# Kernel optimization log

Hardware: AMD Instinct MI355X
Metric: run time of the kernel (lower is better)

## Reference

```python
import jax, jax.numpy as jnp
import numpy as np

RRELU_SLOPE = (1.0 / 8.0 + 1.0 / 3.0) / 2.0  # F.rrelu eval-mode slope
DILATIONS = (1, 2, 4, 8)
HIDDEN_TEMP = 1.0
GUMBEL_TEMP = 0.1


def rrelu(x):
    return jnp.where(x >= 0, x, RRELU_SLOPE * x)


def conv1d(x, w, b, dilation):
    # x: [B, Cin, T], w: [Cout, Cin, K] -> [B, Cout, T'] (VALID, dilated)
    y = jax.lax.conv_general_dilated(
        x, w, window_strides=(1,), padding='VALID', rhs_dilation=(dilation,),
        dimension_numbers=('NCH', 'OIH', 'NCH'))
    return y + b[None, :, None]


def setup_inputs() -> dict:
    key = jax.random.key(0)
    ks = jax.random.split(key, 16)
    B, D, T, R = 8, 32, 4096, 8
    s = 0.05  # param scale for numerical stability
    inp = {
        'x': jax.random.normal(ks[0], (B, D, T), jnp.float32),
        'u': jax.random.uniform(ks[1], (B, T, R), jnp.float32, 1e-6, 1.0 - 1e-6),
        'conv_w0': jax.random.normal(ks[2], (128, D, 2), jnp.float32) * s,
        'conv_b0': jax.random.normal(ks[3], (128,), jnp.float32) * s,
        'conv_w1': jax.random.normal(ks[4], (128, 128, 2), jnp.float32) * s,
        'conv_b1': jax.random.normal(ks[5], (128,), jnp.float32) * s,
        'conv_w2': jax.random.normal(ks[6], (128, 128, 2), jnp.float32) * s,
        'conv_b2': jax.random.normal(ks[7], (128,), jnp.float32) * s,
        'conv_w3': jax.random.normal(ks[8], (R, 128, 2), jnp.float32) * s,
        'conv_b3': jax.random.normal(ks[9], (R,), jnp.float32) * s,
        'pw0': jax.random.normal(ks[10], (R, 256, 128), jnp.float32) * s,
        'pb0': jax.random.normal(ks[11], (R, 256), jnp.float32) * s,
        'pw1': jax.random.normal(ks[12], (R, 2 * D, 256), jnp.float32) * s,
        'pb1': jax.random.normal(ks[13], (R, 2 * D), jnp.float32) * s,
    }
    return inp


def reference(x, u, conv_w0, conv_b0, conv_w1, conv_b1, conv_w2, conv_b2,
              conv_w3, conv_b3, pw0, pb0, pw1, pb1):
    pad = sum(DILATIONS)  # causal left pad
    h = jnp.pad(x, ((0, 0), (0, 0), (pad, 0)))
    for w, b, d in ((conv_w0, conv_b0, DILATIONS[0]),
                    (conv_w1, conv_b1, DILATIONS[1]),
                    (conv_w2, conv_b2, DILATIONS[2])):
        h = rrelu(conv1d(h, w, b, d))
    pre = h  # [B, 128, T + dilations[-1]]
    h_vecs = rrelu(conv1d(pre, conv_w3, conv_b3, DILATIONS[3]))  # [B, R, T]
    pre = pre[:, :, DILATIONS[3]:]  # [B, 128, T]

    p = jax.nn.softmax(h_vecs / HIDDEN_TEMP, axis=1)  # [B, R, T]
    logits = jnp.log(p).transpose(0, 2, 1)  # [B, T, R]
    g = -jnp.log(-jnp.log(u))  # gumbel noise from uniform input
    gen_z = jax.nn.softmax((logits + g) / GUMBEL_TEMP, axis=-1).transpose(0, 2, 1)  # [B, R, T]

    # Fused mixture-of-experts dynamic linear: equal to materializing
    # einsum('brt,roi->boit') then contracting with pre, but avoids the huge tensor.
    params = (jnp.einsum('brt,roi,bit->bot', gen_z, pw0, pre)
              + jnp.einsum('brt,ro->bot', gen_z, pb0))
    # NOTE: original calls F.rrelu(params) without assignment -> no-op (kept faithful)
    params = (jnp.einsum('brt,roi,bit->bot', gen_z, pw1, params)
              + jnp.einsum('brt,ro->bot', gen_z, pb1))

    mus, sig = jnp.split(params, 2, axis=1)  # each [B, n_dims, T]
    sigmas = 0.5 + 0.5 * jnp.tanh(sig) + 0.001
    return mus, sigmas, gen_z
```

## Files before the change

kernel.cpp:

```cpp
#include <hip/hip_runtime.h>
#include <math.h>

typedef __attribute__((ext_vector_type(8))) short bf16x8;
typedef __attribute__((ext_vector_type(4))) float f32x4;
struct __align__(8)  us4 { unsigned short x,y,z,w; };
struct __align__(16) ui4 { unsigned x,y,z,w; };

#define SLOPE 0.2291666666666667f
constexpr int N0=4110, N1=4108, N2=4104, NX=4111;

__device__ __forceinline__ unsigned short f2bf(float f){
  unsigned u = __float_as_uint(f);
  u = (u + 0x7FFF + ((u>>16)&1)) >> 16;
  return (unsigned short)u;
}
__device__ __forceinline__ float bf2f(unsigned short h){
  return __uint_as_float(((unsigned)h)<<16);
}
__device__ __forceinline__ float rrelu(float v){ return v>=0.f ? v : v*SLOPE; }

__global__ __launch_bounds__(256) void prep_w(
  const float* __restrict__ w0, const float* __restrict__ w1, const float* __restrict__ w2,
  const float* __restrict__ pw0, const float* __restrict__ pw1,
  const float* __restrict__ pb0, const float* __restrict__ pb1,
  unsigned short* __restrict__ w0e, unsigned short* __restrict__ w1e, unsigned short* __restrict__ w2e,
  unsigned short* __restrict__ pw0b, unsigned short* __restrict__ pw1b,
  unsigned short* __restrict__ pb0e, unsigned short* __restrict__ pb1e)
{
  int idx = blockIdx.x*256 + threadIdx.x;
  if (idx < 8192){ int oc=idx>>6, k=idx&63, tap=k>>5, i=k&31;
    w0e[idx] = f2bf(w0[(oc*32+i)*2+tap]); return; }
  idx -= 8192;
  if (idx < 32768){ int oc=idx>>8, k=idx&255, tap=k>>7, i=k&127;
    w1e[idx] = f2bf(w1[(oc*128+i)*2+tap]); return; }
  idx -= 32768;
  if (idx < 32768){ int oc=idx>>8, k=idx&255, tap=k>>7, i=k&127;
    w2e[idx] = f2bf(w2[(oc*128+i)*2+tap]); return; }
  idx -= 32768;
  if (idx < 262144){ pw0b[idx] = f2bf(pw0[idx]); return; }
  idx -= 262144;
  if (idx < 131072){ pw1b[idx] = f2bf(pw1[idx]); return; }
  idx -= 131072;
  if (idx < 8192){ int o=idx>>5, r=idx&31; pb0e[idx] = r<8 ? f2bf(pb0[r*256+o]) : (unsigned short)0; return; }
  idx -= 8192;
  if (idx < 2048){ int o=idx>>5, r=idx&31; pb1e[idx] = r<8 ? f2bf(pb1[r*64+o]) : (unsigned short)0; return; }
}

__global__ __launch_bounds__(64) void prep_xt(const float* __restrict__ x,
                                              unsigned short* __restrict__ xt)
{
  __shared__ float s[32][64];
  const int b = blockIdx.y, j0 = blockIdx.x*64, l = threadIdx.x;
  #pragma unroll 4
  for (int i=0;i<32;i++){
    int p = j0 + l - 15;
    s[i][l] = (p>=0 && p<4096) ? x[((size_t)b*32+i)*4096+p] : 0.f;
  }
  __syncthreads();
  const int j = j0 + l;
  if (j < NX){
    unsigned tmp[16];
    #pragma unroll
    for (int q=0;q<16;q++)
      tmp[q] = (unsigned)f2bf(s[2*q][l]) | ((unsigned)f2bf(s[2*q+1][l])<<16);
    ui4* dst = (ui4*)(xt + ((size_t)b*NX + j)*32);
    #pragma unroll
    for (int q=0;q<4;q++){ ui4 v={tmp[4*q],tmp[4*q+1],tmp[4*q+2],tmp[4*q+3]}; dst[q]=v; }
  }
}

template<int IC, int DIL, int NIN, int NOUT>
__global__ __launch_bounds__(256) void conv_g(
    const unsigned short* __restrict__ act,
    const unsigned short* __restrict__ wgt,
    const float* __restrict__ bias,
    unsigned short* __restrict__ outp)
{
  constexpr int KT   = 2*IC;
  constexpr int NK   = KT/32;
  constexpr int NH   = (KT > 128) ? 2 : 1;
  constexpr int KPH  = KT / NH;
  constexpr int NKH  = KPH/32;
  constexpr int HRB  = KPH*2;
  constexpr int HCPR = HRB/16;
  __shared__ __align__(16) char wsm[64*HRB];
  __shared__ __align__(16) char outs[64*128];

  const int tid = threadIdx.x;
  const int b = blockIdx.z, ob = blockIdx.y, tb = blockIdx.x*64;
  const int o0g = ob*64;
  const int wid = tid>>6, l = tid&63, lo = l&15, hi = l>>4;

  bf16x8 bfr[NK];
  {
    const int tg = tb + wid*16 + lo;
    const int te = tg < NOUT ? tg : NOUT-1;
    #pragma unroll
    for (int kk=0;kk<NK;kk++){
      int k = kk*32 + hi*8;
      int tap = (k >= IC) ? 1 : 0;
      int off = k - tap*IC;
      bfr[kk] = *(const bf16x8*)(act + ((size_t)b*NIN + te + tap*DIL)*IC + off);
    }
  }

  f32x4 acc[4];
  #pragma unroll
  for (int m=0;m<4;m++) acc[m] = (f32x4){0.f,0.f,0.f,0.f};

  #pragma unroll
  for (int h=0; h<NH; ++h){
    __syncthreads();
    for (int c = tid; c < 64*HCPR; c += 256){
      int row = c / HCPR, cc = c % HCPR;
      ui4 v = *(const ui4*)((const char*)wgt + (size_t)(o0g+row)*KT*2 + h*HRB + cc*16);
      *(ui4*)(wsm + row*HRB + ((cc*16) ^ ((row&7)<<4))) = v;
    }
    __syncthreads();
    #pragma unroll
    for (int kk=0;kk<NKH;kk++){
      #pragma unroll
      for (int m=0;m<4;m++){
        int row = m*16 + lo;
        bf16x8 af = *(const bf16x8*)(wsm + row*HRB + ((kk*64+hi*16) ^ ((row&7)<<4)));
        acc[m] = __builtin_amdgcn_mfma_f32_16x16x32_bf16(af, bfr[h*NKH+kk], acc[m], 0,0,0);
      }
    }
  }
  __syncthreads();
  #pragma unroll
  for (int m=0;m<4;m++){
    const int ol = m*16 + hi*4;
    float b0v = bias[o0g+ol+0], b1v = bias[o0g+ol+1], b2v = bias[o0g+ol+2], b3v = bias[o0g+ol+3];
    int tl = wid*16 + lo;
    us4 v;
    v.x = f2bf(rrelu(acc[m][0] + b0v));
    v.y = f2bf(rrelu(acc[m][1] + b1v));
    v.z = f2bf(rrelu(acc[m][2] + b2v));
    v.w = f2bf(rrelu(acc[m][3] + b3v));
    *(us4*)(outs + tl*128 + ((ol*2) ^ ((tl&7)<<4))) = v;
  }
  __syncthreads();
  #pragma unroll
  for (int i=0;i<2;i++){
    int c = tid + i*256;
    int row = c>>3, cc = c&7;
    if (tb + row < NOUT){
      ui4 v = *(const ui4*)(outs + row*128 + ((cc*16) ^ ((row&7)<<4)));
      *(ui4*)(outp + ((size_t)b*NOUT + tb + row)*128 + o0g + cc*8) = v;
    }
  }
}

__global__ __launch_bounds__(64) void gumbel_g(
  const unsigned short* __restrict__ h2t,
  const float* __restrict__ w3, const float* __restrict__ b3,
  const float* __restrict__ u,
  float* __restrict__ genz,
  unsigned short* __restrict__ zt)
{
  __shared__ unsigned hs[72][66];
  const int b = blockIdx.y, t0 = blockIdx.x*64, l = threadIdx.x;
  const unsigned* src = (const unsigned*)(h2t + ((size_t)b*N2 + t0)*128);
  for (int e=l; e<72*64; e+=64) hs[e>>6][e&63] = src[e];
  __syncthreads();

  float acc[8];
  #pragma unroll
  for (int r=0;r<8;r++) acc[r]=b3[r];
  for (int i2=0;i2<64;i2++){
    unsigned a0 = hs[l][i2], a1 = hs[l+8][i2];
    float v00 = bf2f(a0&0xffff), v01 = bf2f(a0>>16);
    float v10 = bf2f(a1&0xffff), v11 = bf2f(a1>>16);
    const int i = 2*i2;
    #pragma unroll
    for (int r=0;r<8;r++){
      acc[r] = fmaf(w3[(r*128+i)*2],     v00, acc[r]);
      acc[r] = fmaf(w3[(r*128+i)*2+1],   v10, acc[r]);
      acc[r] = fmaf(w3[(r*128+i+1)*2],   v01, acc[r]);
      acc[r] = fmaf(w3[(r*128+i+1)*2+1], v11, acc[r]);
    }
  }
  float m = -1e30f;
  #pragma unroll
  for (int r=0;r<8;r++){ acc[r] = rrelu(acc[r]); m = fmaxf(m, acc[r]); }
  float s = 0.f;
  #pragma unroll
  for (int r=0;r<8;r++) s += __expf(acc[r]-m);
  const float lse = m + __logf(s);
  const int t = t0 + l;
  const float* ub = u + ((size_t)b*4096 + t)*8;
  float y[8], m2 = -1e30f;
  #pragma unroll
  for (int r=0;r<8;r++){
    float g = -__logf(-__logf(ub[r]));
    y[r] = (acc[r] - lse + g)*10.f;
    m2 = fmaxf(m2, y[r]);
  }
  float s2 = 0.f;
  #pragma unroll
  for (int r=0;r<8;r++){ y[r] = __expf(y[r]-m2); s2 += y[r]; }
  const float inv = 1.f/s2;
  #pragma unroll
  for (int r=0;r<8;r++){
    y[r] *= inv;
    genz[((size_t)b*8+r)*4096 + t] = y[r];
  }
  ui4 zp = { (unsigned)f2bf(y[0]) | ((unsigned)f2bf(y[1])<<16),
             (unsigned)f2bf(y[2]) | ((unsigned)f2bf(y[3])<<16),
             (unsigned)f2bf(y[4]) | ((unsigned)f2bf(y[5])<<16),
             (unsigned)f2bf(y[6]) | ((unsigned)f2bf(y[7])<<16) };
  ui4 zz = {0,0,0,0};
  ui4* zd = (ui4*)(zt + ((size_t)b*4096 + t)*32);
  zd[0]=zp; zd[1]=zz; zd[2]=zz; zd[3]=zz;
}

__global__ __launch_bounds__(256) void moe1_m(
  const unsigned short* __restrict__ h2t,
  const float* __restrict__ genz,
  const unsigned short* __restrict__ zt,
  const unsigned short* __restrict__ pw0b,
  const unsigned short* __restrict__ pb0e,
  unsigned short* __restrict__ hidt)
{
  __shared__ __align__(16) char pres[16384];
  __shared__ __align__(16) char outb[8192];
  __shared__ float zl[512];

  const int ob = blockIdx.x, b = blockIdx.z, tb = blockIdx.y*64;
  const int o0g = ob*64;
  const int tid = threadIdx.x;
  #pragma unroll
  for (int i=0;i<2;i++){
    int e = tid + i*256;
    zl[e] = genz[((size_t)b*8 + (e>>6))*4096 + tb + (e&63)];
  }
  {
    const char* src = (const char*)(h2t + ((size_t)b*N2 + tb + 8)*128);
    #pragma unroll
    for (int i=0;i<4;i++){
      int c = tid + i*256, row = c>>4, cc = c&15;
      ui4 v = *(const ui4*)(src + row*256 + cc*16);
      *(ui4*)(pres + row*256 + ((cc*16) ^ ((row&7)<<4))) = v;
    }
  }
  __syncthreads();

  const int wid = tid>>6, l = tid&63, lo = l&15, hi = l>>4;
  const int ow = o0g + wid*16;

  bf16x8 bfr[4][4];
  #pragma unroll
  for (int n=0;n<4;n++){
    int tl = n*16 + lo;
    #pragma unroll
    for (int kk=0;kk<4;kk++)
      bfr[n][kk] = *(const bf16x8*)(pres + tl*256 + ((kk*64 + hi*16) ^ ((tl&7)<<4)));
  }
  f32x4 acc[4];
  {
    bf16x8 pf = *(const bf16x8*)(pb0e + (size_t)(ow + lo)*32 + hi*8);
    #pragma unroll
    for (int n=0;n<4;n++){
      bf16x8 zf = *(const bf16x8*)(zt + ((size_t)b*4096 + tb + n*16 + lo)*32 + hi*8);
      acc[n] = __builtin_amdgcn_mfma_f32_16x16x32_bf16(pf, zf, (f32x4){0.f,0.f,0.f,0.f}, 0,0,0);
    }
  }

  const unsigned short* abase = pw0b + (size_t)(ow + lo)*128 + hi*8;
  bf16x8 A[4], An[4];
  #pragma unroll
  for (int kk=0;kk<4;kk++) A[kk] = *(const bf16x8*)(abase + kk*32);

  #pragma unroll
  for (int r=0;r<8;r++){
    if (r < 7){
      #pragma unroll
      for (int kk=0;kk<4;kk++)
        An[kk] = *(const bf16x8*)(abase + (size_t)(r+1)*32768 + kk*32);
    }
    f32x4 ar[4];
    #pragma unroll
    for (int n=0;n<4;n++) ar[n] = (f32x4){0.f,0.f,0.f,0.f};
    #pragma unroll
    for (int kk=0;kk<4;kk++)
      #pragma unroll
      for (int n=0;n<4;n++)
        ar[n] = __builtin_amdgcn_mfma_f32_16x16x32_bf16(A[kk], bfr[n][kk], ar[n], 0,0,0);
    #pragma unroll
    for (int n=0;n<4;n++){
      float zv = zl[r*64 + n*16 + lo];
      #pragma unroll
      for (int c2=0;c2<4;c2++)
        acc[n][c2] = fmaf(zv, ar[n][c2], acc[n][c2]);
    }
    if (r < 7){
      #pragma unroll
      for (int kk=0;kk<4;kk++) A[kk] = An[kk];
    }
  }

  #pragma unroll
  for (int n=0;n<4;n++){
    int tl = n*16 + lo;
    int ol2 = (wid*16 + hi*4)*2;
    us4 v;
    v.x=f2bf(acc[n][0]); v.y=f2bf(acc[n][1]); v.z=f2bf(acc[n][2]); v.w=f2bf(acc[n][3]);
    *(us4*)(outb + tl*128 + (ol2 ^ ((tl&7)<<4))) = v;
  }
  __syncthreads();
  #pragma unroll
  for (int i=0;i<2;i++){
    int c = tid + i*256, row = c>>3, cc = c&7;
    ui4 v = *(const ui4*)(outb + row*128 + ((cc*16) ^ ((row&7)<<4)));
    *(ui4*)(hidt + (((size_t)b*4 + ob)*4096 + tb + row)*64 + cc*8) = v;
  }
}

__global__ __launch_bounds__(512) void moe2_m(
  const unsigned short* __restrict__ hidt,
  const float* __restrict__ genz,
  const unsigned short* __restrict__ zt,
  const unsigned short* __restrict__ pw1b,
  const unsigned short* __restrict__ pb1e,
  float* __restrict__ out)
{
  __shared__ __align__(16) char smem[32768*2 + 4096];
  char* abuf0 = smem;
  char* abuf1 = smem + 32768;
  float* zl  = (float*)(smem + 65536);

  const int wg = blockIdx.x;
  const int b = wg >> 5, tb = (wg & 31) * 128;

  const int tid = threadIdx.x;
  #pragma unroll
  for (int i=0;i<2;i++){
    int e = tid + i*512;
    zl[e] = genz[((size_t)b*8 + (e>>7))*4096 + tb + (e&127)];
  }

  const int wid = tid>>6, l = tid&63, lo = l&15, hi = l>>4;
  const int tg = tb + wid*16 + lo;

  bf16x8 bfr[8];
  #pragma unroll
  for (int kk=0;kk<8;kk++)
    bfr[kk] = *(const bf16x8*)(hidt + (((size_t)b*4 + (kk>>1))*4096 + tg)*64 + (kk&1)*32 + hi*8);
  f32x4 acc[4];
  {
    bf16x8 zf = *(const bf16x8*)(zt + ((size_t)b*4096 + tg)*32 + hi*8);
    #pragma unroll
    for (int m=0;m<4;m++){
      bf16x8 pf = *(const bf16x8*)(pb1e + (size_t)(m*16 + lo)*32 + hi*8);
      acc[m] = __builtin_amdgcn_mfma_f32_16x16x32_bf16(pf, zf, (f32x4){0.f,0.f,0.f,0.f}, 0,0,0);
    }
  }

  {
    const char* src = (const char*)pw1b;
    #pragma unroll
    for (int i=0;i<4;i++){
      int c = tid + i*512, row = c>>5, cc = c&31;
      ui4 v = *(const ui4*)(src + row*512 + cc*16);
      *(ui4*)(abuf0 + row*512 + ((cc*16) ^ ((row&7)<<4))) = v;
    }
  }
  __syncthreads();

  #pragma unroll
  for (int r=0;r<8;r++){
    char* cur = (r&1) ? abuf1 : abuf0;
    char* nxt = (r&1) ? abuf0 : abuf1;
    ui4 stg[4];
    if (r < 7){
      const char* src = (const char*)(pw1b + (size_t)(r+1)*16384);
      #pragma unroll
      for (int i=0;i<4;i++){
        int c = tid + i*512;
        stg[i] = *(const ui4*)(src + (c>>5)*512 + (c&31)*16);
      }
    }
    f32x4 ar[4];
    #pragma unroll
    for (int m=0;m<4;m++) ar[m] = (f32x4){0.f,0.f,0.f,0.f};
    #pragma unroll
    for (int kk=0;kk<8;kk++){
      #pragma unroll
      for (int m=0;m<4;m++){
        int row = m*16 + lo;
        int kb  = kk*64 + hi*16;
        bf16x8 af = *(const bf16x8*)(cur + row*512 + (kb ^ ((row&7)<<4)));
        ar[m] = __builtin_amdgcn_mfma_f32_16x16x32_bf16(af, bfr[kk], ar[m], 0,0,0);
      }
    }
    float zv = zl[r*128 + wid*16 + lo];
    #pragma unroll
    for (int m=0;m<4;m++)
      #pragma unroll
      for (int c2=0;c2<4;c2++)
        acc[m][c2] = fmaf(zv, ar[m][c2], acc[m][c2]);
    if (r < 7){
      #pragma unroll
      for (int i=0;i<4;i++){
        int c = tid + i*512;
        *(ui4*)(nxt + (c>>5)*512 + (((c&31)*16) ^ (((c>>5)&7)<<4))) = stg[i];
      }
    }
    __syncthreads();
  }

  #pragma unroll
  for (int m=0;m<4;m++){
    #pragma unroll
    for (int c2=0;c2<4;c2++){
      int o = m*16 + hi*4 + c2;
      float v = acc[m][c2];
      if (o < 32)
        out[((size_t)b*32 + o)*4096 + tg] = v;
      else {
        float e = __expf(2.f*v);
        float th = 1.f - 2.f/(e+1.f);
        out[(size_t)1048576 + ((size_t)b*32 + (o-32))*4096 + tg] = 0.5f + 0.5f*th + 0.001f;
      }
    }
  }
}

extern "C" void kernel_launch(void* const* d_in, const int* in_sizes, int n_in,
                              void* d_out, int out_size, void* d_ws, size_t ws_size,
                              hipStream_t stream) {
  const float* x   = (const float*)d_in[0];
  const float* u   = (const float*)d_in[1];
  const float* w0  = (const float*)d_in[2];
  const float* b0  = (const float*)d_in[3];
  const float* w1  = (const float*)d_in[4];
  const float* b1  = (const float*)d_in[5];
  const float* w2  = (const float*)d_in[6];
  const float* b2  = (const float*)d_in[7];
  const float* w3  = (const float*)d_in[8];
  const float* b3  = (const float*)d_in[9];
  const float* pw0 = (const float*)d_in[10];
  const float* pb0 = (const float*)d_in[11];
  const float* pw1 = (const float*)d_in[12];
  const float* pb1 = (const float*)d_in[13];

  float* out  = (float*)d_out;
  float* genz = out + (size_t)2*8*32*4096;

  char* p = (char*)d_ws;
  unsigned short* xt   = (unsigned short*)p; p += 2104832;
  unsigned short* h0t  = (unsigned short*)p; p += 8417280;
  unsigned short* h1t  = (unsigned short*)p; p += 8413184;
  unsigned short* h2t  = (unsigned short*)p; p += 8404992;
  unsigned short* ztb  = (unsigned short*)p; p += 2097152;
  unsigned short* hidt = (unsigned short*)p; p += 16777216;
  unsigned short* w0e  = (unsigned short*)p; p += 16384;
  unsigned short* w1e  = (unsigned short*)p; p += 65536;
  unsigned short* w2e  = (unsigned short*)p; p += 65536;
  unsigned short* pw0b = (unsigned short*)p; p += 524288;
  unsigned short* pw1b = (unsigned short*)p; p += 262144;
  unsigned short* pb0e = (unsigned short*)p; p += 16384;
  unsigned short* pb1e = (unsigned short*)p; p += 4096;

  prep_w<<<1864, 256, 0, stream>>>(w0,w1,w2,pw0,pw1,pb0,pb1,
                                   w0e,w1e,w2e,pw0b,pw1b,pb0e,pb1e);
  prep_xt<<<dim3(65,8), 64, 0, stream>>>(x, xt);
  conv_g<32,1,NX,N0><<<dim3(65,2,8), 256, 0, stream>>>(xt,  w0e, b0, h0t);
  conv_g<128,2,N0,N1><<<dim3(65,2,8), 256, 0, stream>>>(h0t, w1e, b1, h1t);
  conv_g<128,4,N1,N2><<<dim3(65,2,8), 256, 0, stream>>>(h1t, w2e, b2, h2t);
  gumbel_g<<<dim3(64,8), 64, 0, stream>>>(h2t, w3, b3, u, genz, ztb);
  moe1_m<<<dim3(4,64,8), 256, 0, stream>>>(h2t, genz, ztb, pw0b, pb0e, hidt);
  moe2_m<<<256, 512, 0, stream>>>(hidt, genz, ztb, pw1b, pb1e, out);
}
```

Measured before the change: 132.4 us.

## Restructure moe2 to register-resident expert weights and LDS-staged activations

In moe1, expert-weight fragments are now double-buffered in registers with a distance-two prefetch, alternating between A0 and A1 instead of copying An to A. moe2 is reorganised the same way as moe1. Each wave now holds a 16-row slice of the pw1 expert weights in registers, with two-deep prefetch across experts, and the 64-timestep activation tile is staged once into swizzled LDS. This replaces the old scheme that streamed the full per-expert weight matrix through double-buffered LDS with a barrier every expert. The grid becomes 512 blocks of 256 threads rather than 256 of 512, and the per-expert syncthreads go away. The cost is higher register pressure (16 bf16x8 weight fragments per thread) and repeated LDS reads of activations for every expert.

```diff
diff --git a/kernel.cpp b/kernel.cpp
--- a/kernel.cpp
+++ b/kernel.cpp
@@ -268,35 +268,46 @@
   }
 
   const unsigned short* abase = pw0b + (size_t)(ow + lo)*128 + hi*8;
-  bf16x8 A[4], An[4];
-  #pragma unroll
-  for (int kk=0;kk<4;kk++) A[kk] = *(const bf16x8*)(abase + kk*32);
+  bf16x8 A0[4], A1[4];
+  #pragma unroll
+  for (int kk=0;kk<4;kk++) A0[kk] = *(const bf16x8*)(abase + kk*32);
+  #pragma unroll
+  for (int kk=0;kk<4;kk++) A1[kk] = *(const bf16x8*)(abase + 32768 + kk*32);
 
   #pragma unroll
   for (int r=0;r<8;r++){
-    if (r < 7){
+    f32x4 ar[4];
+    #pragma unroll
+    for (int n=0;n<4;n++) ar[n] = (f32x4){0.f,0.f,0.f,0.f};
+    if ((r&1)==0){
       #pragma unroll
       for (int kk=0;kk<4;kk++)
-        An[kk] = *(const bf16x8*)(abase + (size_t)(r+1)*32768 + kk*32);
-    }
-    f32x4 ar[4];
-    #pragma unroll
-    for (int n=0;n<4;n++) ar[n] = (f32x4){0.f,0.f,0.f,0.f};
-    #pragma unroll
-    for (int kk=0;kk<4;kk++)
-      #pragma unroll
-      for (int n=0;n<4;n++)
-        ar[n] = __builtin_amdgcn_mfma_f32_16x16x32_bf16(A[kk], bfr[n][kk], ar[n], 0,0,0);
+        #pragma unroll
+        for (int n=0;n<4;n++)
+          ar[n] = __builtin_amdgcn_mfma_f32_16x16x32_bf16(A0[kk], bfr[n][kk], ar[n], 0,0,0);
+      if (r < 6){
+        #pragma unroll
+        for (int kk=0;kk<4;kk++)
+          A0[kk] = *(const bf16x8*)(abase + (size_t)(r+2)*32768 + kk*32);
+      }
+    } else {
+      #pragma unroll
+      for (int kk=0;kk<4;kk++)
+        #pragma unroll
+        for (int n=0;n<4;n++)
+          ar[n] = __builtin_amdgcn_mfma_f32_16x16x32_bf16(A1[kk], bfr[n][kk], ar[n], 0,0,0);
+      if (r < 6){
+        #pragma unroll
+        for (int kk=0;kk<4;kk++)
+          A1[kk] = *(const bf16x8*)(abase + (size_t)(r+2)*32768 + kk*32);
+      }
+    }
     #pragma unroll
     for (int n=0;n<4;n++){
       float zv = zl[r*64 + n*16 + lo];
       #pragma unroll
       for (int c2=0;c2<4;c2++)
         acc[n][c2] = fmaf(zv, ar[n][c2], acc[n][c2]);
-    }
-    if (r < 7){
-      #pragma unroll
-      for (int kk=0;kk<4;kk++) A[kk] = An[kk];
     }
   }
 
@@ -317,7 +328,7 @@
   }
 }
 
-__global__ __launch_bounds__(512) void moe2_m(
+__global__ __launch_bounds__(256) void moe2_m(
   const unsigned short* __restrict__ hidt,
   const float* __restrict__ genz,
   const unsigned short* __restrict__ zt,
@@ -325,103 +336,103 @@
   const unsigned short* __restrict__ pb1e,
   float* __restrict__ out)
 {
-  __shared__ __align__(16) char smem[32768*2 + 4096];
-  char* abuf0 = smem;
-  char* abuf1 = smem + 32768;
-  float* zl  = (float*)(smem + 65536);
-
-  const int wg = blockIdx.x;
-  const int b = wg >> 5, tb = (wg & 31) * 128;
-
+  __shared__ __align__(16) char hids[32768];
+  __shared__ float zl[512];
+
+  const int b = blockIdx.y, tb = blockIdx.x*64;
   const int tid = threadIdx.x;
   #pragma unroll
   for (int i=0;i<2;i++){
-    int e = tid + i*512;
-    zl[e] = genz[((size_t)b*8 + (e>>7))*4096 + tb + (e&127)];
-  }
+    int e = tid + i*256;
+    zl[e] = genz[((size_t)b*8 + (e>>6))*4096 + tb + (e&63)];
+  }
+  #pragma unroll
+  for (int i=0;i<8;i++){
+    int c = tid + i*256, row = c>>5, cc = c&31;
+    int obq = cc>>3, wi = cc&7;
+    ui4 v = *(const ui4*)(hidt + (((size_t)b*4 + obq)*4096 + tb + row)*64 + wi*8);
+    *(ui4*)(hids + row*512 + ((cc*16) ^ ((row&7)<<4))) = v;
+  }
+  __syncthreads();
 
   const int wid = tid>>6, l = tid&63, lo = l&15, hi = l>>4;
-  const int tg = tb + wid*16 + lo;
-
-  bf16x8 bfr[8];
-  #pragma unroll
-  for (int kk=0;kk<8;kk++)
-    bfr[kk] = *(const bf16x8*)(hidt + (((size_t)b*4 + (kk>>1))*4096 + tg)*64 + (kk&1)*32 + hi*8);
+  const int ow = wid*16;
+
   f32x4 acc[4];
   {
-    bf16x8 zf = *(const bf16x8*)(zt + ((size_t)b*4096 + tg)*32 + hi*8);
-    #pragma unroll
-    for (int m=0;m<4;m++){
-      bf16x8 pf = *(const bf16x8*)(pb1e + (size_t)(m*16 + lo)*32 + hi*8);
-      acc[m] = __builtin_amdgcn_mfma_f32_16x16x32_bf16(pf, zf, (f32x4){0.f,0.f,0.f,0.f}, 0,0,0);
-    }
-  }
-
-  {
-    const char* src = (const char*)pw1b;
-    #pragma unroll
-    for (int i=0;i<4;i++){
-      int c = tid + i*512, row = c>>5, cc = c&31;
-      ui4 v = *(const ui4*)(src + row*512 + cc*16);
-      *(ui4*)(abuf0 + row*512 + ((cc*16) ^ ((row&7)<<4))) = v;
-    }
-  }
-  __syncthreads();
+    bf16x8 pf = *(const bf16x8*)(pb1e + (size_t)(ow + lo)*32 + hi*8);
+    #pragma unroll
+    for (int n=0;n<4;n++){
+      bf16x8 zf = *(const bf16x8*)(zt + ((size_t)b*4096 + tb + n*16 + lo)*32 + hi*8);
+      acc[n] = __builtin_amdgcn_mfma_f32_16x16x32_bf16(pf, zf, (f32x4){0.f,0.f,0.f,0.f}, 0,0,0);
+    }
+  }
+
+  const unsigned short* abase = pw1b + (size_t)(ow + lo)*256 + hi*8;
+  bf16x8 A0[8], A1[8];
+  #pragma unroll
+  for (int kk=0;kk<8;kk++) A0[kk] = *(const bf16x8*)(abase + kk*32);
+  #pragma unroll
+  for (int kk=0;kk<8;kk++) A1[kk] = *(const bf16x8*)(abase + 16384 + kk*32);
 
   #pragma unroll
   for (int r=0;r<8;r++){
-    char* cur = (r&1) ? abuf1 : abuf0;
-    char* nxt = (r&1) ? abuf0 : abuf1;
-    ui4 stg[4];
-    if (r < 7){
-      const char* src = (const char*)(pw1b + (size_t)(r+1)*16384);
-      #pragma unroll
-      for (int i=0;i<4;i++){
-        int c = tid + i*512;
-        stg[i] = *(const ui4*)(src + (c>>5)*512 + (c&31)*16);
-      }
-    }
     f32x4 ar[4];
     #pragma unroll
-    for (int m=0;m<4;m++) ar[m] = (f32x4){0.f,0.f,0.f,0.f};
-    #pragma unroll
-    for (int kk=0;kk<8;kk++){
-      #pragma unroll
-      for (int m=0;m<4;m++){
-        int row = m*16 + lo;
-        int kb  = kk*64 + hi*16;
-        bf16x8 af = *(const bf16x8*)(cur + row*512 + (kb ^ ((row&7)<<4)));
-        ar[m] = __builtin_amdgcn_mfma_f32_16x16x32_bf16(af, bfr[kk], ar[m], 0,0,0);
-      }
-    }
-    float zv = zl[r*128 + wid*16 + lo];
-    #pragma unroll
-    for (int m=0;m<4;m++)
+    for (int n=0;n<4;n++) ar[n] = (f32x4){0.f,0.f,0.f,0.f};
+    if ((r&1)==0){
+      #pragma unroll
+      for (int kk=0;kk<8;kk++){
+        #pragma unroll
+        for (int n=0;n<4;n++){
+          int tl = n*16 + lo;
+          bf16x8 bf = *(const bf16x8*)(hids + tl*512 + ((kk*64 + hi*16) ^ ((tl&7)<<4)));
+          ar[n] = __builtin_amdgcn_mfma_f32_16x16x32_bf16(A0[kk], bf, ar[n], 0,0,0);
+        }
+      }
+      if (r < 6){
+        #pragma unroll
+        for (int kk=0;kk<8;kk++)
+          A0[kk] = *(const bf16x8*)(abase + (size_t)(r+2)*16384 + kk*32);
+      }
+    } else {
+      #pragma unroll
+      for (int kk=0;kk<8;kk++){
+        #pragma unroll
+        for (int n=0;n<4;n++){
+          int tl = n*16 + lo;
+          bf16x8 bf = *(const bf16x8*)(hids + tl*512 + ((kk*64 + hi*16) ^ ((tl&7)<<4)));
+          ar[n] = __builtin_amdgcn_mfma_f32_16x16x32_bf16(A1[kk], bf, ar[n], 0,0,0);
+        }
+      }
+      if (r < 6){
+        #pragma unroll
+        for (int kk=0;kk<8;kk++)
+          A1[kk] = *(const bf16x8*)(abase + (size_t)(r+2)*16384 + kk*32);
+      }
+    }
+    #pragma unroll
+    for (int n=0;n<4;n++){
+      float zv = zl[r*64 + n*16 + lo];
       #pragma unroll
       for (int c2=0;c2<4;c2++)
-        acc[m][c2] = fmaf(zv, ar[m][c2], acc[m][c2]);
-    if (r < 7){
-      #pragma unroll
-      for (int i=0;i<4;i++){
-        int c = tid + i*512;
-        *(ui4*)(nxt + (c>>5)*512 + (((c&31)*16) ^ (((c>>5)&7)<<4))) = stg[i];
-      }
-    }
-    __syncthreads();
-  }
-
-  #pragma unroll
-  for (int m=0;m<4;m++){
+        acc[n][c2] = fmaf(zv, ar[n][c2], acc[n][c2]);
+    }
+  }
+
+  #pragma unroll
+  for (int n=0;n<4;n++){
+    int t = tb + n*16 + lo;
     #pragma unroll
     for (int c2=0;c2<4;c2++){
-      int o = m*16 + hi*4 + c2;
-      float v = acc[m][c2];
+      int o = ow + hi*4 + c2;
+      float v = acc[n][c2];
       if (o < 32)
-        out[((size_t)b*32 + o)*4096 + tg] = v;
+        out[((size_t)b*32 + o)*4096 + t] = v;
       else {
         float e = __expf(2.f*v);
         float th = 1.f - 2.f/(e+1.f);
-        out[(size_t)1048576 + ((size_t)b*32 + (o-32))*4096 + tg] = 0.5f + 0.5f*th + 0.001f;
+        out[(size_t)1048576 + ((size_t)b*32 + (o-32))*4096 + t] = 0.5f + 0.5f*th + 0.001f;
       }
     }
   }
@@ -471,5 +482,5 @@
   conv_g<128,4,N1,N2><<<dim3(65,2,8), 256, 0, stream>>>(h1t, w2e, b2, h2t);
   gumbel_g<<<dim3(64,8), 64, 0, stream>>>(h2t, w3, b3, u, genz, ztb);
   moe1_m<<<dim3(4,64,8), 256, 0, stream>>>(h2t, genz, ztb, pw0b, pb0e, hidt);
-  moe2_m<<<256, 512, 0, stream>>>(hidt, genz, ztb, pw1b, pb1e, out);
-}
+  moe2_m<<<dim3(64,8), 256, 0, stream>>>(hidt, genz, ztb, pw1b, pb1e, out);
+}
```

After: 136.9 us. +3.4%, slower.
